# Kernel optimization log

Measured on AMD Instinct MI355X. Metric: run time of the kernel, lower is better.

The kernel has to match this reference:

```python
import jax, jax.numpy as jnp
import numpy as np

B, S, V, E, H = 32, 64, 32000, 300, 1024


def setup_inputs() -> dict:
    key = jax.random.key(0)
    ks = jax.random.split(key, 16)
    s = 0.05
    inp = {
        "sent": jax.random.randint(ks[0], (B, S), 0, V),
        "length": jax.random.randint(ks[1], (B,), 2, S + 1),
        "emb": jax.random.normal(ks[2], (V, E), jnp.float32) * s,
        # layer 0: input E -> H ; layer 1: H -> H. PyTorch GRUCell layout [3H, in].
        "Wi0": jax.random.normal(ks[3], (3 * H, E), jnp.float32) * s,
        "Wh0": jax.random.normal(ks[4], (3 * H, H), jnp.float32) * s,
        "bi0": jnp.zeros((3 * H,), jnp.float32),
        "bh0": jnp.zeros((3 * H,), jnp.float32),
        "Wi1": jax.random.normal(ks[5], (3 * H, H), jnp.float32) * s,
        "Wh1": jax.random.normal(ks[6], (3 * H, H), jnp.float32) * s,
        "bi1": jnp.zeros((3 * H,), jnp.float32),
        "bh1": jnp.zeros((3 * H,), jnp.float32),
        "Wout": jax.random.normal(ks[7], (V, H), jnp.float32) * s,
        "bout": jnp.zeros((V,), jnp.float32),
    }
    return inp


def gru_step(x, h, Wi, Wh, bi, bh):
    gx = x @ Wi.T + bi            # [B, 3H]
    gh = h @ Wh.T + bh            # [B, 3H]
    rx, zx, nx = jnp.split(gx, 3, axis=-1)
    rh, zh, nh = jnp.split(gh, 3, axis=-1)
    r = jax.nn.sigmoid(rx + rh)
    z = jax.nn.sigmoid(zx + zh)
    n = jnp.tanh(nx + r * nh)
    return (1.0 - z) * n + z * h


def reference(sent, length, emb, Wi0, Wh0, bi0, bh0, Wi1, Wh1, bi1, bh1, Wout, bout):
    x = emb[sent]                              # [B, S, E]
    xs = jnp.swapaxes(x[:, : S - 1], 0, 1)     # [S-1, B, E]

    def step(carry, x_t):
        h0, h1 = carry
        h0 = gru_step(x_t, h0, Wi0, Wh0, bi0, bh0)
        h1 = gru_step(h0, h1, Wi1, Wh1, bi1, bh1)
        return (h0, h1), h1

    h_init = (jnp.zeros((B, H), x.dtype), jnp.zeros((B, H), x.dtype))
    _, hs = jax.lax.scan(step, h_init, xs)     # hs: [S-1, B, H]

    logits = jnp.einsum("sbh,vh->bsv", hs, Wout) + bout   # [B, S-1, V]
    logp = jax.nn.log_softmax(logits, axis=-1)
    targets = sent[:, 1:]                                   # [B, S-1]
    tok_logp = jnp.take_along_axis(logp, targets[:, :, None], axis=2)[..., 0]
    len_ng = length - 1                                     # [B]
    mask = jnp.arange(S - 1)[None, :] < len_ng[:, None]
    tok_logp = tok_logp * mask.astype(tok_logp.dtype)
    loss_batch = -jnp.sum(tok_logp, axis=1) / len_ng.astype(tok_logp.dtype)
    loss = jnp.mean(loss_batch)
    return loss, logits
```

## Files before the change

kernel.cpp:

```cpp
#include <hip/hip_runtime.h>

typedef unsigned short u16;
typedef unsigned int u32;
typedef unsigned long long u64;
typedef _Float16 f16;
typedef __attribute__((ext_vector_type(8))) __bf16 bf16x8;
typedef __attribute__((ext_vector_type(8))) _Float16 f16x8;
typedef __attribute__((ext_vector_type(4))) _Float16 f16x4;
typedef __attribute__((ext_vector_type(4))) float f32x4;

#define DEVI static __device__ __forceinline__

#define BB 32
#define SS 64
#define TT 63
#define VV 32000
#define EE 300
#define EP 320
#define HH 1024
#define H3 3072
#define MM 2016
#define MP 2048
#define NWG 192
#define NWG_TOT 256
#define NT 250

DEVI u16 f2bf(float f) {
  u32 x = __float_as_uint(f);
  u32 r = x + 0x7FFFu + ((x >> 16) & 1u);
  return (u16)(r >> 16);
}
DEVI float bf2f(u16 h) { return __uint_as_float(((u32)h) << 16); }
DEVI float sigm(float x) { return 1.0f / (1.0f + __expf(-x)); }
DEVI float tanh_(float x) { return 2.0f / (1.0f + __expf(-2.0f * x)) - 1.0f; }

DEVI void gl_lds16(const void* g, void* l) {
  __builtin_amdgcn_global_load_lds((const __attribute__((address_space(1))) void*)g,
                                   (__attribute__((address_space(3))) void*)l,
                                   16, 0, 0);
}

DEVI f32x4 mfma_bf16(bf16x8 a, bf16x8 b, f32x4 c) {
  return __builtin_amdgcn_mfma_f32_16x16x32_bf16(a, b, c, 0, 0, 0);
}
DEVI f32x4 mfma_f16(f16x8 a, f16x8 b, f32x4 c) {
  return __builtin_amdgcn_mfma_f32_16x16x32_f16(a, b, c, 0, 0, 0);
}

DEVI f16x8 frag_ld(const f16* base, int kk, int kg, int brow) {
  const u64* q = (const u64*)base;
  int i0 = (kk * 8 + kg * 2) * 32 + brow;
  union { u64 u[2]; f16x8 v; } t;
  t.u[0] = __hip_atomic_load(q + i0, __ATOMIC_RELAXED, __HIP_MEMORY_SCOPE_AGENT);
  t.u[1] = __hip_atomic_load(q + i0 + 32, __ATOMIC_RELAXED, __HIP_MEMORY_SCOPE_AGENT);
  return t.v;
}
DEVI void ast32(u32* p, u32 v) {
  __hip_atomic_store(p, v, __ATOMIC_RELAXED, __HIP_MEMORY_SCOPE_AGENT);
}
DEVI u32 ald32(const u32* p) {
  return __hip_atomic_load(p, __ATOMIC_RELAXED, __HIP_MEMORY_SCOPE_AGENT);
}
DEVI u32* frag_wslot(f16* base, int j0, int b) {
  return (u32*)((char*)base + ((j0 >> 2) * 256 + b * 8 + (j0 & 3) * 2));
}

DEVI void gbar(u32* flags, int wg, u32 target) {
  __syncthreads();
  if (threadIdx.x == 0) ast32(&flags[wg * 16], target);
  int ok;
  do {
    u32 v = (threadIdx.x < NWG) ? ald32(&flags[threadIdx.x * 16]) : target;
    ok = (v >= target);
  } while (__syncthreads_and(ok) == 0);
}


__global__ void cvt3_f16(const float* __restrict__ s0, const float* __restrict__ s1,
                         const float* __restrict__ s2, f16* __restrict__ dst0) {
  const int seg = H3 * HH / 4;
  int i = blockIdx.x * 256 + threadIdx.x;
  int stride = gridDim.x * 256;
  for (; i < 3 * seg; i += stride) {
    int which = i / seg, off = i - which * seg;
    const float* s = (which == 0) ? s0 : (which == 1) ? s1 : s2;
    float4 v = ((const float4*)s)[off];
    f16x4 o = {(f16)v.x, (f16)v.y, (f16)v.z, (f16)v.w};
    ((f16x4*)dst0)[i] = o;
  }
}

__global__ void cvt_wi0_f16(const float* __restrict__ W, f16* __restrict__ out) {
  int i = blockIdx.x * 256 + threadIdx.x;
  int stride = gridDim.x * 256;
  for (; i < H3 * EP; i += stride) {
    int r = i / EP, c = i % EP;
    out[i] = (c < EE) ? (f16)W[(size_t)r * EE + c] : (f16)0.0f;
  }
}

__global__ void gather_x_f16(const int* __restrict__ sent, const float* __restrict__ emb,
                             f16* __restrict__ xf) {
  int i = blockIdx.x * 256 + threadIdx.x;
  int stride = gridDim.x * 256;
  for (; i < MM * EP; i += stride) {
    int m = i / EP, c = i % EP;
    int t = m >> 5, b = m & 31;
    int tok = sent[b * SS + t];
    xf[i] = (c < EE) ? (f16)emb[(size_t)tok * EE + c] : (f16)0.0f;
  }
}


template <bool REMAP, bool XSWZ>
__global__ __launch_bounds__(256) void gemm_bt(const u16* __restrict__ Ah, int lda,
                                               const u16* __restrict__ Bh,
                                               const float* __restrict__ bias,
                                               float* __restrict__ out, int out_stride,
                                               int Ksteps, int Mtiles, int Mvalid,
                                               float* __restrict__ pmg,
                                               float* __restrict__ psg) {
  __shared__ u16 As[128 * 64];
  __shared__ u16 Bs[128 * 64];
  __shared__ float pm[128][2], ps[128][2];
  int bid = blockIdx.x;
  if (XSWZ) bid = (bid & 7) * (gridDim.x >> 3) + (bid >> 3);
  const int mtile = bid % Mtiles, ntile = bid / Mtiles;
  const int tid = threadIdx.x;
  const int lane = tid & 63, wave = tid >> 6;
  const int wrow = (wave & 1) * 64, wcol = (wave >> 1) * 64;
  const int l15 = lane & 15, kg = lane >> 4;

  f32x4 acc[4][4];
#pragma unroll
  for (int i = 0; i < 4; ++i)
#pragma unroll
    for (int j = 0; j < 4; ++j) {
      f32x4 z = {0.f, 0.f, 0.f, 0.f};
      acc[i][j] = z;
    }

  for (int ks = 0; ks < Ksteps; ++ks) {
    int k0 = ks * 64;
#pragma unroll
    for (int it = 0; it < 4; ++it) {
      int c = it * 256 + tid;
      int r = c >> 3, kc = (c & 7) * 8;
      gl_lds16(Ah + (size_t)(mtile * 128 + r) * lda + k0 + kc, &As[c * 8]);
      gl_lds16(Bh + (size_t)(ntile * 128 + r) * lda + k0 + kc, &Bs[c * 8]);
    }
    __syncthreads();
#pragma unroll
    for (int kk = 0; kk < 2; ++kk) {
      bf16x8 ah[4], bh[4];
#pragma unroll
      for (int i = 0; i < 4; ++i) {
        ah[i] = *(const bf16x8*)&As[(wrow + i * 16 + l15) * 64 + kk * 32 + kg * 8];
        bh[i] = *(const bf16x8*)&Bs[(wcol + i * 16 + l15) * 64 + kk * 32 + kg * 8];
      }
#pragma unroll
      for (int i = 0; i < 4; ++i)
#pragma unroll
        for (int j = 0; j < 4; ++j) acc[i][j] = mfma_bf16(ah[i], bh[j], acc[i][j]);
    }
    __syncthreads();
  }

  float bv4[4];
#pragma unroll
  for (int j = 0; j < 4; ++j) bv4[j] = bias[ntile * 128 + wcol + j * 16 + l15];

  const int r0 = kg * 4;
#pragma unroll
  for (int i = 0; i < 4; ++i) {
    int mbase = mtile * 128 + wrow + i * 16 + r0;
#pragma unroll
    for (int j = 0; j < 4; ++j) {
      int n = ntile * 128 + wcol + j * 16 + l15;
#pragma unroll
      for (int reg = 0; reg < 4; ++reg) {
        int m = mbase + reg;
        if (m < Mvalid) {
          float v = acc[i][j][reg] + bv4[j];
          size_t oidx;
          if (REMAP) {
            int b = m & 31, s = m >> 5;
            oidx = ((size_t)(b * TT + s)) * VV + n;
          } else {
            oidx = (size_t)m * out_stride + n;
          }
          out[oidx] = v;
        }
      }
    }
  }

  if constexpr (REMAP) {
#pragma unroll
    for (int i = 0; i < 4; ++i) {
#pragma unroll
      for (int reg = 0; reg < 4; ++reg) {
        float v0 = acc[i][0][reg] + bv4[0];
        float v1 = acc[i][1][reg] + bv4[1];
        float v2 = acc[i][2][reg] + bv4[2];
        float v3 = acc[i][3][reg] + bv4[3];
        float rm = fmaxf(fmaxf(v0, v1), fmaxf(v2, v3));
#pragma unroll
        for (int off = 1; off < 16; off <<= 1) rm = fmaxf(rm, __shfl_xor(rm, off));
        float sm = __expf(v0 - rm) + __expf(v1 - rm) + __expf(v2 - rm) +
                   __expf(v3 - rm);
#pragma unroll
        for (int off = 1; off < 16; off <<= 1) sm += __shfl_xor(sm, off);
        if (l15 == 0) {
          int r128 = wrow + i * 16 + kg * 4 + reg;
          pm[r128][wcol >> 6] = rm;
          ps[r128][wcol >> 6] = sm;
        }
      }
    }
    __syncthreads();
    if (tid < 128) {
      int m = mtile * 128 + tid;
      if (m < Mvalid) {
        float m0 = pm[tid][0], m1 = pm[tid][1];
        float s0 = ps[tid][0], s1 = ps[tid][1];
        float mn = fmaxf(m0, m1);
        float ss = s0 * __expf(m0 - mn) + s1 * __expf(m1 - mn);
        int b = m & 31, s = m >> 5;
        size_t rr = (size_t)(b * TT + s);
        pmg[(size_t)ntile * MM + rr] = mn;
        psg[(size_t)ntile * MM + rr] = ss;
      }
    }
  }
}

__global__ __launch_bounds__(256) void gemm_bt_f16(const f16* __restrict__ A, int lda,
                                                   const f16* __restrict__ B,
                                                   const float* __restrict__ bias,
                                                   float* __restrict__ out, int out_stride,
                                                   int Ksteps, int Mtiles, int Mvalid) {
  __shared__ f16 As[128 * 64];
  __shared__ f16 Bs[128 * 64];
  const int bid = blockIdx.x;
  const int mtile = bid % Mtiles, ntile = bid / Mtiles;
  const int tid = threadIdx.x;
  const int lane = tid & 63, wave = tid >> 6;
  const int wrow = (wave & 1) * 64, wcol = (wave >> 1) * 64;
  const int l15 = lane & 15, kg = lane >> 4;

  f32x4 acc[4][4];
#pragma unroll
  for (int i = 0; i < 4; ++i)
#pragma unroll
    for (int j = 0; j < 4; ++j) {
      f32x4 z = {0.f, 0.f, 0.f, 0.f};
      acc[i][j] = z;
    }

  for (int ks = 0; ks < Ksteps; ++ks) {
    int k0 = ks * 64;
#pragma unroll
    for (int it = 0; it < 4; ++it) {
      int c = it * 256 + tid;
      int r = c >> 3, kc = (c & 7) * 8;
      gl_lds16(A + (size_t)(mtile * 128 + r) * lda + k0 + kc, &As[c * 8]);
      gl_lds16(B + (size_t)(ntile * 128 + r) * lda + k0 + kc, &Bs[c * 8]);
    }
    __syncthreads();
#pragma unroll
    for (int kk = 0; kk < 2; ++kk) {
      f16x8 a[4], b[4];
#pragma unroll
      for (int i = 0; i < 4; ++i) {
        a[i] = *(const f16x8*)&As[(wrow + i * 16 + l15) * 64 + kk * 32 + kg * 8];
        b[i] = *(const f16x8*)&Bs[(wcol + i * 16 + l15) * 64 + kk * 32 + kg * 8];
      }
#pragma unroll
      for (int i = 0; i < 4; ++i)
#pragma unroll
        for (int j = 0; j < 4; ++j) acc[i][j] = mfma_f16(a[i], b[j], acc[i][j]);
    }
    __syncthreads();
  }

  const int r0 = kg * 4;
#pragma unroll
  for (int i = 0; i < 4; ++i) {
    int mbase = mtile * 128 + wrow + i * 16 + r0;
#pragma unroll
    for (int j = 0; j < 4; ++j) {
      int n = ntile * 128 + wcol + j * 16 + l15;
      float bv = bias[n];
#pragma unroll
      for (int reg = 0; reg < 4; ++reg) {
        int m = mbase + reg;
        if (m < Mvalid) {
          out[(size_t)m * out_stride + n] = acc[i][j][reg] + bv;
        }
      }
    }
  }
}


struct RecArgs {
  const f16 *wh0, *wi1, *wh1;
  const float *gx0, *bh0, *bi1, *bh1;
  f16 *h0x, *h1x;
  u16 *hs;
  u32 *bar;
  const float *wout;
  u16 *woutb;
};

__global__ __launch_bounds__(1024, 1) void rec_kernel(RecArgs ra) {
  __shared__ f16 wlds[48 * 1024];
  __shared__ float gh[4 * 48 * 33];
  const int tid = threadIdx.x;
  const int wg = blockIdx.x;

  if (wg >= NWG) {
    int i = (wg - NWG) * 1024 + tid;
    const int stride = (NWG_TOT - NWG) * 1024;
    for (; i < VV * HH / 4; i += stride) {
      float4 v = ((const float4*)ra.wout)[i];
      ushort4 o;
      o.x = f2bf(v.x); o.y = f2bf(v.y); o.z = f2bf(v.z); o.w = f2bf(v.w);
      ((ushort4*)ra.woutb)[i] = o;
    }
    return;
  }

  const int lane = tid & 63, wave = tid >> 6;
  const bool isL0 = wg < 64;
  const int Jbase = isL0 ? (wg * 16) : ((wg - 64) * 8);
  const int l15 = lane & 15;
  const int kg = lane >> 4;
  const int swz = (l15 & 7) << 4;
  const int kh = wave >> 2;
  const int khk = kh * 8;
  float* ghk = gh + kh * (48 * 33);
  char* wb = (char*)wlds;

#pragma unroll
  for (int it = 0; it < 6; ++it) {
    int q = it * 1024 + tid;
    int r = q >> 7;
    int c16 = q & 127;
    const f16* gp;
    if (isL0) {
      int gate = r >> 4, colr = r & 15;
      gp = ra.wh0 + ((size_t)(gate * HH + Jbase + colr)) * HH + c16 * 8;
    } else {
      int tile = r >> 3, colr = r & 7;
      int msrc = tile / 3, gate = tile - msrc * 3;
      const f16* W = msrc ? ra.wh1 : ra.wi1;
      gp = W + ((size_t)(gate * HH + Jbase + colr)) * HH + c16 * 8;
    }
    f16x8 v = *(const f16x8*)gp;
    int byte = r * 2048 + ((c16 * 16) ^ ((r & 7) << 4));
    *(f16x8*)(wb + byte) = v;
  }

  const int ewb = tid & 31, ewj = tid >> 5;
  float hprev = 0.f;
  float pb0r = 0.f, pb0z = 0.f, pb0n = 0.f;
  float pbrz_r = 0.f, pbrz_z = 0.f, pbn_i = 0.f, pbn_h = 0.f;
  if (isL0 && tid < 512) {
    int gj = Jbase + ewj;
    pb0r = ra.bh0[gj];
    pb0z = ra.bh0[HH + gj];
    pb0n = ra.bh0[2 * HH + gj];
  } else if (!isL0 && tid < 256) {
    int gj = Jbase + ewj;
    pbrz_r = ra.bi1[gj] + ra.bh1[gj];
    pbrz_z = ra.bi1[HH + gj] + ra.bh1[HH + gj];
    pbn_i = ra.bi1[2 * HH + gj];
    pbn_h = ra.bh1[2 * HH + gj];
  }
  __syncthreads();

  for (int p = 0; p < 64; ++p) {
    const int pb = p & 1, qb = (p + 1) & 1;
    if (isL0) {
      if (p < TT) {
        float gr = 0.f, gz = 0.f, gn = 0.f;
        if (tid < 512) {
          const float* gxb = ra.gx0 + ((size_t)p * BB + ewb) * H3;
          int gj = Jbase + ewj;
          gr = gxb[gj];
          gz = gxb[HH + gj];
          gn = gxb[2 * HH + gj];
        }
        const int rt = (wave >> 1) & 1, tt = wave & 1;
        const f16* h0base = ra.h0x + (size_t)qb * (BB * HH);
        const int brow = rt * 16 + l15;
        f32x4 z = {0.f, 0.f, 0.f, 0.f};
        if (tt == 0) {
          f32x4 acc0 = z, acc1 = z;
#pragma unroll 4
          for (int ki = 0; ki < 8; ++ki) {
            int kk = khk + ki;
            f16x8 a = frag_ld(h0base, kk, kg, brow);
            int inner = (kk * 64 + kg * 16) ^ swz;
            f16x8 b0 = *(const f16x8*)(wb + (0 * 16 + l15) * 2048 + inner);
            f16x8 b1 = *(const f16x8*)(wb + (1 * 16 + l15) * 2048 + inner);
            acc0 = mfma_f16(a, b0, acc0);
            acc1 = mfma_f16(a, b1, acc1);
          }
#pragma unroll
          for (int r = 0; r < 4; ++r) {
            ghk[(l15)*33 + rt * 16 + kg * 4 + r] = acc0[r];
            ghk[(16 + l15) * 33 + rt * 16 + kg * 4 + r] = acc1[r];
          }
        } else {
          f32x4 acc2 = z;
#pragma unroll 4
          for (int ki = 0; ki < 8; ++ki) {
            int kk = khk + ki;
            f16x8 a = frag_ld(h0base, kk, kg, brow);
            int inner = (kk * 64 + kg * 16) ^ swz;
            f16x8 b2 = *(const f16x8*)(wb + (2 * 16 + l15) * 2048 + inner);
            acc2 = mfma_f16(a, b2, acc2);
          }
#pragma unroll
          for (int r = 0; r < 4; ++r)
            ghk[(32 + l15) * 33 + rt * 16 + kg * 4 + r] = acc2[r];
        }
        __syncthreads();
        if (tid < 512) {
          f16* hxc = ra.h0x + (size_t)pb * (BB * HH);
          float rh = pb0r, zh = pb0z, nh = pb0n;
#pragma unroll
          for (int g = 0; g < 4; ++g) {
            rh += gh[g * (48 * 33) + (ewj)*33 + ewb];
            zh += gh[g * (48 * 33) + (16 + ewj) * 33 + ewb];
            nh += gh[g * (48 * 33) + (32 + ewj) * 33 + ewb];
          }
          float r = sigm(gr + rh);
          float zz = sigm(gz + zh);
          float n = tanh_(gn + r * nh);
          float hn = (1.f - zz) * n + zz * hprev;
          hprev = hn;
          float other = __shfl_xor(hn, 32);
          if ((lane & 32) == 0) {
            union { f16 h[2]; u32 u; } pk;
            pk.h[0] = (f16)hn;
            pk.h[1] = (f16)other;
            ast32(frag_wslot(hxc, Jbase + ewj, ewb), pk.u);
          }
        }
      } else {
        __syncthreads();
      }
    } else {
      if (p >= 1) {
        const int rt = (wave >> 1) & 1, src = wave & 1;
        const f16* hbase = (src ? ra.h1x : ra.h0x) + (size_t)qb * (BB * HH);
        const int brow = rt * 16 + l15;
        const int rowb = src * 24 + (l15 & 7);
        f32x4 z = {0.f, 0.f, 0.f, 0.f};
        f32x4 acc0 = z, acc1 = z, acc2 = z;
#pragma unroll 4
        for (int ki = 0; ki < 8; ++ki) {
          int kk = khk + ki;
          f16x8 a = frag_ld(hbase, kk, kg, brow);
          int inner = (kk * 64 + kg * 16) ^ swz;
          f16x8 b0 = *(const f16x8*)(wb + (rowb + 0) * 2048 + inner);
          f16x8 b1 = *(const f16x8*)(wb + (rowb + 8) * 2048 + inner);
          f16x8 b2 = *(const f16x8*)(wb + (rowb + 16) * 2048 + inner);
          acc0 = mfma_f16(a, b0, acc0);
          acc1 = mfma_f16(a, b1, acc1);
          acc2 = mfma_f16(a, b2, acc2);
        }
        if (l15 < 8) {
          f32x4 accs[3] = {acc0, acc1, acc2};
#pragma unroll
          for (int g = 0; g < 3; ++g) {
            int cl = (src * 3 + g) * 8 + l15;
#pragma unroll
            for (int r = 0; r < 4; ++r)
              ghk[cl * 33 + rt * 16 + kg * 4 + r] = accs[g][r];
          }
        }
        __syncthreads();
        if (tid < 256) {
          f16* hxc = ra.h1x + (size_t)pb * (BB * HH);
          float gir = 0.f, giz = 0.f, gin = 0.f, ghr = 0.f, ghz = 0.f, ghn = 0.f;
#pragma unroll
          for (int g = 0; g < 4; ++g) {
            const float* gg = gh + g * (48 * 33);
            gir += gg[(ewj)*33 + ewb];
            giz += gg[(8 + ewj) * 33 + ewb];
            gin += gg[(16 + ewj) * 33 + ewb];
            ghr += gg[(24 + ewj) * 33 + ewb];
            ghz += gg[(32 + ewj) * 33 + ewb];
            ghn += gg[(40 + ewj) * 33 + ewb];
          }
          float r = sigm(gir + ghr + pbrz_r);
          float zz = sigm(giz + ghz + pbrz_z);
          float n = tanh_(gin + pbn_i + r * (ghn + pbn_h));
          float hn = (1.f - zz) * n + zz * hprev;
          hprev = hn;
          float other = __shfl_xor(hn, 32);
          if ((lane & 32) == 0) {
            union { f16 h[2]; u32 u; } pk;
            pk.h[0] = (f16)hn;
            pk.h[1] = (f16)other;
            ast32(frag_wslot(hxc, Jbase + ewj, ewb), pk.u);
            union { u16 h[2]; u32 u; } pb2;
            pb2.h[0] = f2bf(hn);
            pb2.h[1] = f2bf(other);
            *(u32*)&ra.hs[((size_t)(p - 1) * BB + ewb) * HH + Jbase + ewj] = pb2.u;
          }
        }
      } else {
        __syncthreads();
      }
    }
    if (p < 63) gbar(ra.bar, wg, (u32)(p + 1));
  }
}


__global__ __launch_bounds__(256) void rowred2_kernel(const float* __restrict__ pmg,
                                                      const float* __restrict__ psg,
                                                      const float* __restrict__ logits,
                                                      const int* __restrict__ sent,
                                                      const int* __restrict__ length,
                                                      float* __restrict__ tok) {
  __shared__ float redm[4], reds[4];
  const int row = blockIdx.x;
  const int b = row / TT, s = row % TT;
  const int tid = threadIdx.x;
  const int lane = tid & 63, wave = tid >> 6;

  float m = -1e30f, sum = 0.f;
  if (tid < NT) {
    m = pmg[(size_t)tid * MM + row];
    sum = psg[(size_t)tid * MM + row];
  }
  for (int off = 1; off < 64; off <<= 1) {
    float mo = __shfl_xor(m, off);
    float so = __shfl_xor(sum, off);
    float mn = fmaxf(m, mo);
    sum = sum * __expf(m - mn) + so * __expf(mo - mn);
    m = mn;
  }
  if (lane == 0) {
    redm[wave] = m;
    reds[wave] = sum;
  }
  __syncthreads();
  if (tid == 0) {
    float M = redm[0], S = reds[0];
#pragma unroll
    for (int w = 1; w < 4; ++w) {
      float mo = redm[w], so = reds[w];
      float mn = fmaxf(M, mo);
      S = S * __expf(M - mn) + so * __expf(mo - mn);
      M = mn;
    }
    float lse = M + __logf(S);
    int tgt = sent[b * SS + s + 1];
    float tl = logits[(size_t)row * VV + tgt] - lse;
    if (s >= length[b] - 1) tl = 0.f;
    tok[row] = tl;
  }
}

__global__ void loss_kernel(const float* __restrict__ tok, const int* __restrict__ length,
                            float* __restrict__ out0) {
  int lane = threadIdx.x;
  float v = 0.f;
  if (lane < BB) {
    float s = 0.f;
    for (int t = 0; t < TT; ++t) s += tok[lane * TT + t];
    float ln = (float)(length[lane] - 1);
    v = -s / ln;
  }
  v += __shfl_down(v, 16);
  v += __shfl_down(v, 8);
  v += __shfl_down(v, 4);
  v += __shfl_down(v, 2);
  v += __shfl_down(v, 1);
  if (lane == 0) out0[0] = v / (float)BB;
}


extern "C" void kernel_launch(void* const* d_in, const int* in_sizes, int n_in,
                              void* d_out, int out_size, void* d_ws, size_t ws_size,
                              hipStream_t stream) {
  const int* sent = (const int*)d_in[0];
  const int* length = (const int*)d_in[1];
  const float* emb = (const float*)d_in[2];
  const float* Wi0 = (const float*)d_in[3];
  const float* Wh0 = (const float*)d_in[4];
  const float* bi0 = (const float*)d_in[5];
  const float* bh0 = (const float*)d_in[6];
  const float* Wi1 = (const float*)d_in[7];
  const float* Wh1 = (const float*)d_in[8];
  const float* bi1 = (const float*)d_in[9];
  const float* bh1 = (const float*)d_in[10];
  const float* Wout = (const float*)d_in[11];
  const float* bout = (const float*)d_in[12];
  float* out = (float*)d_out;

  char* ws = (char*)d_ws;
  size_t off = 0;
  auto alloc = [&](size_t b) {
    char* p = ws + off;
    off = (off + b + 255) & ~(size_t)255;
    return p;
  };
  f16* wh0f = (f16*)alloc((size_t)H3 * HH * 2);
  f16* wi1f = (f16*)alloc((size_t)H3 * HH * 2);
  f16* wh1f = (f16*)alloc((size_t)H3 * HH * 2);
  f16* wi0f = (f16*)alloc((size_t)H3 * EP * 2);
  f16* xf = (f16*)alloc((size_t)MP * EP * 2);
  float* gx0 = (float*)alloc((size_t)MM * H3 * 4);
  u16* woutb = (u16*)alloc((size_t)VV * HH * 2);
  u16* hs = (u16*)alloc((size_t)MP * HH * 2);
  f16* h0x = (f16*)alloc((size_t)2 * BB * HH * 2);
  f16* h1x = (f16*)alloc((size_t)2 * BB * HH * 2);
  float* tok = (float*)alloc((size_t)MM * 4);
  u32* bar = (u32*)alloc((size_t)NWG * 16 * 4);
  float* pmg = (float*)alloc((size_t)MM * NT * 4);
  float* psg = (float*)alloc((size_t)MM * NT * 4);

  hipMemsetAsync(h0x, 0, (size_t)2 * BB * HH * 2, stream);
  hipMemsetAsync(h1x, 0, (size_t)2 * BB * HH * 2, stream);
  hipMemsetAsync(hs, 0, (size_t)MP * HH * 2, stream);
  hipMemsetAsync(bar, 0, (size_t)NWG * 16 * 4, stream);
  hipMemsetAsync(xf + (size_t)MM * EP, 0, (size_t)(MP - MM) * EP * 2, stream);

  cvt3_f16<<<2048, 256, 0, stream>>>(Wh0, Wi1, Wh1, wh0f);
  cvt_wi0_f16<<<512, 256, 0, stream>>>(Wi0, wi0f);
  gather_x_f16<<<512, 256, 0, stream>>>(sent, emb, xf);

  gemm_bt_f16<<<16 * 24, 256, 0, stream>>>(xf, EP, wi0f, bi0, gx0, H3, 5, 16, MM);

  RecArgs ra{wh0f, wi1f, wh1f, gx0, bh0, bi1, bh1, h0x, h1x, hs, bar, Wout, woutb};
  void* kargs[] = {(void*)&ra};
  hipLaunchCooperativeKernel((void*)rec_kernel, dim3(NWG_TOT), dim3(1024), kargs, 0,
                             stream);

  gemm_bt<true, true><<<16 * 250, 256, 0, stream>>>(hs, HH, woutb, bout, out + 1, VV, 16,
                                                    16, MM, pmg, psg);

  rowred2_kernel<<<MM, 256, 0, stream>>>(pmg, psg, out + 1, sent, length, tok);
  loss_kernel<<<1, 64, 0, stream>>>(tok, length, out);
}
```

Baseline: 738.8 us.

## Convert recurrent weights to f16 inside rec_kernel and merge front prep kernels

Drops the separate pass that converted Wh0, Wi1 and Wh1 to f16 in global memory. The recurrent kernel now reads the fp32 weights directly and converts them while staging its LDS-resident slice. The Wi0 conversion and the embedding gather are also merged into one launch split by block index. This removes a full read/write pass over about 36 MB of weights plus two launches, at the cost of doubling the bytes each recurrent workgroup loads during its one-time prologue.

```diff
diff --git a/kernel.cpp b/kernel.cpp
--- a/kernel.cpp
+++ b/kernel.cpp
@@ -76,38 +76,25 @@
 }
 
 
-__global__ void cvt3_f16(const float* __restrict__ s0, const float* __restrict__ s1,
-                         const float* __restrict__ s2, f16* __restrict__ dst0) {
-  const int seg = H3 * HH / 4;
-  int i = blockIdx.x * 256 + threadIdx.x;
-  int stride = gridDim.x * 256;
-  for (; i < 3 * seg; i += stride) {
-    int which = i / seg, off = i - which * seg;
-    const float* s = (which == 0) ? s0 : (which == 1) ? s1 : s2;
-    float4 v = ((const float4*)s)[off];
-    f16x4 o = {(f16)v.x, (f16)v.y, (f16)v.z, (f16)v.w};
-    ((f16x4*)dst0)[i] = o;
-  }
-}
-
-__global__ void cvt_wi0_f16(const float* __restrict__ W, f16* __restrict__ out) {
-  int i = blockIdx.x * 256 + threadIdx.x;
-  int stride = gridDim.x * 256;
-  for (; i < H3 * EP; i += stride) {
-    int r = i / EP, c = i % EP;
-    out[i] = (c < EE) ? (f16)W[(size_t)r * EE + c] : (f16)0.0f;
-  }
-}
-
-__global__ void gather_x_f16(const int* __restrict__ sent, const float* __restrict__ emb,
-                             f16* __restrict__ xf) {
-  int i = blockIdx.x * 256 + threadIdx.x;
-  int stride = gridDim.x * 256;
-  for (; i < MM * EP; i += stride) {
-    int m = i / EP, c = i % EP;
-    int t = m >> 5, b = m & 31;
-    int tok = sent[b * SS + t];
-    xf[i] = (c < EE) ? (f16)emb[(size_t)tok * EE + c] : (f16)0.0f;
+__global__ void prep_front(const float* __restrict__ Wi0, f16* __restrict__ wi0f,
+                           const int* __restrict__ sent, const float* __restrict__ emb,
+                           f16* __restrict__ xf) {
+  if (blockIdx.x < 512) {
+    int i = blockIdx.x * 256 + threadIdx.x;
+    const int stride = 512 * 256;
+    for (; i < H3 * EP; i += stride) {
+      int r = i / EP, c = i % EP;
+      wi0f[i] = (c < EE) ? (f16)Wi0[(size_t)r * EE + c] : (f16)0.0f;
+    }
+  } else {
+    int i = (blockIdx.x - 512) * 256 + threadIdx.x;
+    const int stride = 512 * 256;
+    for (; i < MM * EP; i += stride) {
+      int m = i / EP, c = i % EP;
+      int t = m >> 5, b = m & 31;
+      int tok = sent[b * SS + t];
+      xf[i] = (c < EE) ? (f16)emb[(size_t)tok * EE + c] : (f16)0.0f;
+    }
   }
 }
 
@@ -305,7 +292,7 @@
 
 
 struct RecArgs {
-  const f16 *wh0, *wi1, *wh1;
+  const float *wh0, *wi1, *wh1;
   const float *gx0, *bh0, *bi1, *bh1;
   f16 *h0x, *h1x;
   u16 *hs;
@@ -348,17 +335,20 @@
     int q = it * 1024 + tid;
     int r = q >> 7;
     int c16 = q & 127;
-    const f16* gp;
+    const float* gp;
     if (isL0) {
       int gate = r >> 4, colr = r & 15;
       gp = ra.wh0 + ((size_t)(gate * HH + Jbase + colr)) * HH + c16 * 8;
     } else {
       int tile = r >> 3, colr = r & 7;
       int msrc = tile / 3, gate = tile - msrc * 3;
-      const f16* W = msrc ? ra.wh1 : ra.wi1;
+      const float* W = msrc ? ra.wh1 : ra.wi1;
       gp = W + ((size_t)(gate * HH + Jbase + colr)) * HH + c16 * 8;
     }
-    f16x8 v = *(const f16x8*)gp;
+    float4 lo = ((const float4*)gp)[0];
+    float4 hi = ((const float4*)gp)[1];
+    f16x8 v = {(f16)lo.x, (f16)lo.y, (f16)lo.z, (f16)lo.w,
+               (f16)hi.x, (f16)hi.y, (f16)hi.z, (f16)hi.w};
     int byte = r * 2048 + ((c16 * 16) ^ ((r & 7) << 4));
     *(f16x8*)(wb + byte) = v;
   }
@@ -614,9 +604,6 @@
     off = (off + b + 255) & ~(size_t)255;
     return p;
   };
-  f16* wh0f = (f16*)alloc((size_t)H3 * HH * 2);
-  f16* wi1f = (f16*)alloc((size_t)H3 * HH * 2);
-  f16* wh1f = (f16*)alloc((size_t)H3 * HH * 2);
   f16* wi0f = (f16*)alloc((size_t)H3 * EP * 2);
   f16* xf = (f16*)alloc((size_t)MP * EP * 2);
   float* gx0 = (float*)alloc((size_t)MM * H3 * 4);
@@ -635,13 +622,11 @@
   hipMemsetAsync(bar, 0, (size_t)NWG * 16 * 4, stream);
   hipMemsetAsync(xf + (size_t)MM * EP, 0, (size_t)(MP - MM) * EP * 2, stream);
 
-  cvt3_f16<<<2048, 256, 0, stream>>>(Wh0, Wi1, Wh1, wh0f);
-  cvt_wi0_f16<<<512, 256, 0, stream>>>(Wi0, wi0f);
-  gather_x_f16<<<512, 256, 0, stream>>>(sent, emb, xf);
+  prep_front<<<1024, 256, 0, stream>>>(Wi0, wi0f, sent, emb, xf);
 
   gemm_bt_f16<<<16 * 24, 256, 0, stream>>>(xf, EP, wi0f, bi0, gx0, H3, 5, 16, MM);
 
-  RecArgs ra{wh0f, wi1f, wh1f, gx0, bh0, bi1, bh1, h0x, h1x, hs, bar, Wout, woutb};
+  RecArgs ra{Wh0, Wi1, Wh1, gx0, bh0, bi1, bh1, h0x, h1x, hs, bar, Wout, woutb};
   void* kargs[] = {(void*)&ra};
   hipLaunchCooperativeKernel((void*)rec_kernel, dim3(NWG_TOT), dim3(1024), kargs, 0,
                              stream);
```

Result: no change. 728.7 us (-1.4%).
